# Optimization experiments

Measured on AMD Instinct MI355X. Metric: run time of the kernel, lower is better.

## Reference

```python
import jax, jax.numpy as jnp
import numpy as np

# distilled LLaVA-style decoder: nf4-quantized linears + LoRA(q/k/v/o) + gumbel-softmax -> embedding einsum
B, S, D, H, L = 1, 2048, 2048, 16, 2
DH = D // H
DFF, V, R, BLK = 8192, 32000, 8, 64
LORA_SCALE = 16.0 / R  # alpha / r
TAU = 1.0
SQRT_DH = float(np.sqrt(DH))

# bitsandbytes NF4 codebook (16 values)
NF4 = jnp.array([-1.0, -0.6961928009986877, -0.5250730514526367, -0.39491748809814453,
                 -0.28444138169288635, -0.18477343022823334, -0.09105003625154495, 0.0,
                 0.07958029955625534, 0.16093020141124725, 0.24611230194568634,
                 0.33791524171829224, 0.44070982933044434, 0.5626170039176941,
                 0.7229568362236023, 1.0], dtype=jnp.float32)


def dequant(idx, scale):
    # idx [..., out, in] int in [0,16); scale [..., out, in//BLK] per-block absmax
    return NF4[idx] * jnp.repeat(scale, BLK, axis=-1)


def rmsnorm(x, w):
    return x * jax.lax.rsqrt(jnp.mean(x * x, axis=-1, keepdims=True) + 1e-6) * w


def setup_inputs():
    key = jax.random.key(0)
    k = jax.random.split(key, 12)
    return {
        "input_ids": jax.random.randint(k[0], (B, S), 0, V, dtype=jnp.int32),
        "u": jax.random.uniform(k[1], (B, S, V), dtype=jnp.float32),
        "emb": jax.random.normal(k[2], (V, D), dtype=jnp.float32) * 0.02,
        "attn_scale": jax.random.uniform(k[3], (L, 4, D, D // BLK), minval=0.005, maxval=0.02, dtype=jnp.float32),
        "ffn_gu_scale": jax.random.uniform(k[4], (L, 2, DFF, D // BLK), minval=0.005, maxval=0.02, dtype=jnp.float32),
        "ffn_d_scale": jax.random.uniform(k[5], (L, D, DFF // BLK), minval=0.005, maxval=0.02, dtype=jnp.float32),
        "lora_A": jax.random.normal(k[6], (L, 4, R, D), dtype=jnp.float32) * 0.01,
        "lora_B": jax.random.normal(k[7], (L, 4, D, R), dtype=jnp.float32) * 0.01,
        "norm_w": jnp.ones((L, 2, D), dtype=jnp.float32),
        "final_norm_w": jnp.ones((D,), dtype=jnp.float32),
        "attn_idx": jax.random.randint(k[8], (L, 4, D, D), 0, 16, dtype=jnp.int32),
        "ffn_gu_idx": jax.random.randint(k[9], (L, 2, DFF, D), 0, 16, dtype=jnp.int32),
        "ffn_d_idx": jax.random.randint(k[10], (L, D, DFF), 0, 16, dtype=jnp.int32),
    }


def reference(input_ids, u, emb, attn_scale, ffn_gu_scale, ffn_d_scale,
              lora_A, lora_B, norm_w, final_norm_w, attn_idx, ffn_gu_idx, ffn_d_idx):
    h = emb[input_ids]  # [B, S, D]
    causal = jnp.tril(jnp.ones((S, S), dtype=bool))
    for l in range(L):
        x = rmsnorm(h, norm_w[l, 0])
        w = dequant(attn_idx[l], attn_scale[l])  # [4, D, D] dequantized q/k/v/o weights

        def proj(i, t):
            # nf4 linear + LoRA adapter (y = t W^T + (t A^T) B^T * alpha/r)
            return t @ w[i].T + ((t @ lora_A[l, i].T) @ lora_B[l, i].T) * LORA_SCALE

        q = proj(0, x).reshape(B, S, H, DH)
        k_ = proj(1, x).reshape(B, S, H, DH)
        v = proj(2, x).reshape(B, S, H, DH)
        scores = jnp.einsum('bqhd,bkhd->bhqk', q, k_) / SQRT_DH
        scores = jnp.where(causal, scores, -1e30)
        p = jax.nn.softmax(scores, axis=-1)
        o = jnp.einsum('bhqk,bkhd->bqhd', p, v).reshape(B, S, D)
        h = h + proj(3, o)

        x = rmsnorm(h, norm_w[l, 1])
        wgu = dequant(ffn_gu_idx[l], ffn_gu_scale[l])  # [2, DFF, D] gate/up
        wd = dequant(ffn_d_idx[l], ffn_d_scale[l])     # [D, DFF] down
        h = h + (jax.nn.silu(x @ wgu[0].T) * (x @ wgu[1].T)) @ wd.T

    h = rmsnorm(h, final_norm_w)
    logits = h @ emb.T  # [B, S, V]
    # gumbel_softmax(tau, hard=False): softmax((logits + G)/tau), G = -log(-log(U))
    gnoise = -jnp.log(-jnp.log(u + 1e-10) + 1e-10)
    g = jax.nn.softmax((logits + gnoise) / TAU, axis=-1)
    soft_embeddings = jnp.einsum('bsv,vd->bsd', g, emb)
    return soft_embeddings, logits
```

## Files before the change

### kernel.cpp

```cpp
#include <hip/hip_runtime.h>
#include <hip/hip_bf16.h>

typedef unsigned short u16;
typedef unsigned int u32;
typedef __bf16 bf16t;
typedef bf16t bf16x8 __attribute__((ext_vector_type(8)));
typedef float f32x4 __attribute__((ext_vector_type(4)));

constexpr int S_   = 2048;
constexpr int D_   = 2048;
constexpr int H_   = 16;
constexpr int DH_  = 128;
constexpr int L_   = 2;
constexpr int DFF_ = 8192;
constexpr int V_   = 32000;
constexpr int R_   = 8;

__constant__ float c_nf4[16] = {
  -1.0f, -0.6961928009986877f, -0.5250730514526367f, -0.39491748809814453f,
  -0.28444138169288635f, -0.18477343022823334f, -0.09105003625154495f, 0.0f,
  0.07958029955625534f, 0.16093020141124725f, 0.24611230194568634f,
  0.33791524171829224f, 0.44070982933044434f, 0.5626170039176941f,
  0.7229568362236023f, 1.0f };

__device__ __forceinline__ u16 f2bf(float f) {
  union { float f; u32 u; } v; v.f = f;
  u32 r = v.u + 0x7fffu + ((v.u >> 16) & 1u);
  return (u16)(r >> 16);
}
__device__ __forceinline__ float bf2f(u16 h) {
  union { u32 u; float f; } v; v.u = ((u32)h) << 16; return v.f;
}

__global__ __launch_bounds__(256) void k_gather(const int* __restrict__ ids,
                                                const float* __restrict__ emb,
                                                float* __restrict__ h) {
  int t = blockIdx.x * 256 + threadIdx.x;
  int s = t >> 11;
  int d = t & 2047;
  h[t] = emb[(size_t)ids[s] * D_ + d];
}

__global__ __launch_bounds__(256) void k_rmsnorm(const float* __restrict__ in,
                                                 const float* __restrict__ w,
                                                 u16* __restrict__ out) {
  int s = blockIdx.x;
  const float* x = in + (size_t)s * D_;
  float ss = 0.f;
  for (int d = threadIdx.x; d < D_; d += 256) { float v = x[d]; ss += v * v; }
#pragma unroll
  for (int m = 1; m < 64; m <<= 1) ss += __shfl_xor(ss, m, 64);
  __shared__ float sh[4];
  if ((threadIdx.x & 63) == 0) sh[threadIdx.x >> 6] = ss;
  __syncthreads();
  ss = sh[0] + sh[1] + sh[2] + sh[3];
  float sc = rsqrtf(ss * (1.0f / D_) + 1e-6f);
  u16* o = out + (size_t)s * D_;
  for (int d = threadIdx.x; d < D_; d += 256) o[d] = f2bf(x[d] * sc * w[d]);
}

__global__ __launch_bounds__(256) void k_dequant(const int* __restrict__ idx,
                                                 const float* __restrict__ scale,
                                                 u16* __restrict__ out, int kshift) {
  size_t t = (size_t)blockIdx.x * 256 + threadIdx.x;
  size_t e = t * 8;
  int k = (int)(e & ((1u << kshift) - 1));
  size_t n = e >> kshift;
  float s = scale[(n << (kshift - 6)) + (k >> 6)];
  int4 i0 = *(const int4*)(idx + e);
  int4 i1 = *(const int4*)(idx + e + 4);
  uint4 o;
  o.x = (u32)f2bf(c_nf4[i0.x] * s) | ((u32)f2bf(c_nf4[i0.y] * s) << 16);
  o.y = (u32)f2bf(c_nf4[i0.z] * s) | ((u32)f2bf(c_nf4[i0.w] * s) << 16);
  o.z = (u32)f2bf(c_nf4[i1.x] * s) | ((u32)f2bf(c_nf4[i1.y] * s) << 16);
  o.w = (u32)f2bf(c_nf4[i1.z] * s) | ((u32)f2bf(c_nf4[i1.w] * s) << 16);
  *(uint4*)(out + e) = o;
}

__global__ __launch_bounds__(256) void k_f2b(const float* __restrict__ src,
                                             u16* __restrict__ dst) {
  size_t e = ((size_t)blockIdx.x * 256 + threadIdx.x) * 8;
  float4 f0 = *(const float4*)(src + e);
  float4 f1 = *(const float4*)(src + e + 4);
  uint4 o;
  o.x = (u32)f2bf(f0.x) | ((u32)f2bf(f0.y) << 16);
  o.y = (u32)f2bf(f0.z) | ((u32)f2bf(f0.w) << 16);
  o.z = (u32)f2bf(f1.x) | ((u32)f2bf(f1.y) << 16);
  o.w = (u32)f2bf(f1.z) | ((u32)f2bf(f1.w) << 16);
  *(uint4*)(dst + e) = o;
}

__global__ __launch_bounds__(256) void k_transpose(const float* __restrict__ src,
                                                   u16* __restrict__ dst) {
  __shared__ u16 tile[64][65];
  int v0 = blockIdx.x * 64, d0 = blockIdx.y * 64;
  int tid = threadIdx.x;
  int rr = tid >> 4, cc = (tid & 15) * 4;
#pragma unroll
  for (int j = 0; j < 4; ++j) {
    int r = j * 16 + rr;
    float4 f = *(const float4*)(src + (size_t)(v0 + r) * D_ + d0 + cc);
    tile[r][cc + 0] = f2bf(f.x); tile[r][cc + 1] = f2bf(f.y);
    tile[r][cc + 2] = f2bf(f.z); tile[r][cc + 3] = f2bf(f.w);
  }
  __syncthreads();
#pragma unroll
  for (int j = 0; j < 4; ++j) {
    int r = j * 16 + rr;
    ushort4 w;
    w.x = tile[cc + 0][r]; w.y = tile[cc + 1][r];
    w.z = tile[cc + 2][r]; w.w = tile[cc + 3][r];
    *(ushort4*)(dst + (size_t)(d0 + r) * V_ + v0 + cc) = w;
  }
}

enum { OUT_F32 = 0, OUT_F32_ACC = 1, OUT_BF16 = 2 };

template<int OUTMODE>
__global__ __launch_bounds__(512, 2) void k_gemm256(const u16* __restrict__ A, int lda,
                                                    const u16* __restrict__ B, int ldb,
                                                    void* __restrict__ Cv, int ldc,
                                                    int Kc, size_t zstride) {
  __shared__ u16 As[2][256][64];
  __shared__ u16 Bs[2][256][64];
  const int tid = threadIdx.x;
  const int lane = tid & 63, w = tid >> 6;
  const int wr = w >> 2, wc = w & 3;
  const int g = (lane >> 4), l15 = lane & 15, sl7 = lane & 7;

  const int nbx = gridDim.x;
  const int cpx = (nbx * gridDim.y) >> 3;
  int lin = blockIdx.y * nbx + blockIdx.x;
  int swz = (lin & 7) * cpx + (lin >> 3);
  const int m0 = (swz / nbx) * 256;
  const int n0 = (swz % nbx) * 256;

  A += (size_t)blockIdx.z * Kc;
  B += (size_t)blockIdx.z * Kc;
  float* Cf = (float*)Cv + (size_t)blockIdx.z * zstride;

  const int NT = Kc >> 6;
  const int srow = w * 8 + (lane >> 3);
  const int sch  = (lane & 7) ^ (lane >> 3);

  auto stageA = [&](int half, int tile) {
    const u16* src = A + (size_t)(m0 + half * 128 + srow) * lda + tile * 64 + sch * 8;
    u16* dst = &As[tile & 1][half * 128 + w * 8][0];
#pragma unroll
    for (int rnd = 0; rnd < 2; ++rnd)
      __builtin_amdgcn_global_load_lds(
          (const __attribute__((address_space(1))) void*)(src + (size_t)rnd * 64 * lda),
          (__attribute__((address_space(3))) void*)(dst + rnd * 64 * 64), 16, 0, 0);
  };
  auto stageB = [&](int half, int tile) {
    const u16* src = B + (size_t)(n0 + half * 128 + srow) * ldb + tile * 64 + sch * 8;
    u16* dst = &Bs[tile & 1][half * 128 + w * 8][0];
#pragma unroll
    for (int rnd = 0; rnd < 2; ++rnd)
      __builtin_amdgcn_global_load_lds(
          (const __attribute__((address_space(1))) void*)(src + (size_t)rnd * 64 * ldb),
          (__attribute__((address_space(3))) void*)(dst + rnd * 64 * 64), 16, 0, 0);
  };

  f32x4 acc[8][4] = {};
  bf16x8 areg[4][2], breg[2][2][2];

  stageB(0, 0); stageA(0, 0); stageB(1, 0); stageA(1, 0);
  if (NT > 1) {
    stageB(0, 1); stageA(0, 1);
    asm volatile("s_waitcnt vmcnt(4)" ::: "memory");
  } else {
    asm volatile("s_waitcnt vmcnt(0)" ::: "memory");
  }
  __builtin_amdgcn_s_barrier();

#define LOADA(QR)                                                                   \
  _Pragma("unroll") for (int m = 0; m < 4; ++m)                                     \
    _Pragma("unroll") for (int kh = 0; kh < 2; ++kh) {                              \
      int hr = wr * 128 + (QR) * 64 + m * 16 + l15;                                 \
      areg[m][kh] = *(const bf16x8*)(abase + hr * 64 + ((((kh << 2) | g) ^ sl7) << 3)); \
    }
#define LOADB(QC)                                                                   \
  _Pragma("unroll") for (int n = 0; n < 2; ++n)                                     \
    _Pragma("unroll") for (int kh = 0; kh < 2; ++kh) {                              \
      int br = wc * 64 + (QC) * 32 + n * 16 + l15;                                  \
      breg[QC][n][kh] = *(const bf16x8*)(bbase + br * 64 + ((((kh << 2) | g) ^ sl7) << 3)); \
    }
#define QPHASE(QR, QC)                                                              \
  __builtin_amdgcn_s_setprio(1);                                                    \
  _Pragma("unroll") for (int m = 0; m < 4; ++m)                                     \
    _Pragma("unroll") for (int n = 0; n < 2; ++n)                                   \
      _Pragma("unroll") for (int kh = 0; kh < 2; ++kh)                              \
        acc[(QR) * 4 + m][(QC) * 2 + n] = __builtin_amdgcn_mfma_f32_16x16x32_bf16(  \
            areg[m][kh], breg[QC][n][kh], acc[(QR) * 4 + m][(QC) * 2 + n], 0, 0, 0); \
  __builtin_amdgcn_s_setprio(0);

  for (int t = 0; t < NT; ++t) {
    const u16* abase = &As[t & 1][0][0];
    const u16* bbase = &Bs[t & 1][0][0];
    LOADA(0); LOADB(0);
    if (t + 1 < NT) stageB(1, t + 1);
    QPHASE(0, 0);
    __builtin_amdgcn_s_barrier();
    LOADB(1);
    if (t + 1 < NT) stageA(1, t + 1);
    QPHASE(0, 1);
    __builtin_amdgcn_s_barrier();
    LOADA(1);
    if (t + 2 < NT) stageB(0, t + 2);
    QPHASE(1, 1);
    __builtin_amdgcn_s_barrier();
    if (t + 2 < NT) stageA(0, t + 2);
    QPHASE(1, 0);
    if (t + 1 < NT) {
      if (t + 1 == NT - 1) asm volatile("s_waitcnt vmcnt(0)" ::: "memory");
      else                 asm volatile("s_waitcnt vmcnt(4)" ::: "memory");
    }
    __builtin_amdgcn_s_barrier();
  }
#undef LOADA
#undef LOADB
#undef QPHASE

  const int er = g * 4;
#pragma unroll
  for (int i = 0; i < 8; ++i)
#pragma unroll
    for (int j = 0; j < 4; ++j)
#pragma unroll
      for (int r = 0; r < 4; ++r) {
        int row = m0 + wr * 128 + i * 16 + er + r;
        int col = n0 + wc * 64 + j * 16 + l15;
        if (OUTMODE == OUT_BF16) {
          ((u16*)Cv)[(size_t)row * ldc + col] = f2bf(acc[i][j][r]);
        } else if (OUTMODE == OUT_F32_ACC) {
          Cf[(size_t)row * ldc + col] += acc[i][j][r];
        } else {
          Cf[(size_t)row * ldc + col] = acc[i][j][r];
        }
      }
}

__global__ __launch_bounds__(256) void k_red(const float* __restrict__ P,
                                             float* __restrict__ dst, int accmode) {
  size_t i = ((size_t)blockIdx.x * 256 + threadIdx.x) * 4;
  const size_t n = (size_t)4 * 1024 * 1024;
  float4 a = *(const float4*)(P + i);
  float4 b = *(const float4*)(P + n + i);
  float4 c = *(const float4*)(P + 2 * n + i);
  float4 d = *(const float4*)(P + 3 * n + i);
  float4 r;
  r.x = (a.x + b.x) + (c.x + d.x);
  r.y = (a.y + b.y) + (c.y + d.y);
  r.z = (a.z + b.z) + (c.z + d.z);
  r.w = (a.w + b.w) + (c.w + d.w);
  if (accmode) {
    float4 o = *(const float4*)(dst + i);
    r.x += o.x; r.y += o.y; r.z += o.z; r.w += o.w;
  }
  *(float4*)(dst + i) = r;
}

__global__ __launch_bounds__(256) void k_lora_down(const u16* __restrict__ X,
                                                   const float* __restrict__ A,
                                                   float* __restrict__ T, int nproj) {
  int s = blockIdx.x;
  int lane = threadIdx.x & 63, wv = threadIdx.x >> 6;
  const u16* x = X + (size_t)s * D_;
  for (int p = wv; p < nproj * R_; p += 4) {
    const float* a = A + (size_t)p * D_;
    float sum = 0.f;
    for (int d = lane; d < D_; d += 64) sum += bf2f(x[d]) * a[d];
#pragma unroll
    for (int m = 1; m < 64; m <<= 1) sum += __shfl_xor(sum, m, 64);
    if (lane == 0) T[(size_t)s * (nproj * R_) + p] = sum;
  }
}

__global__ __launch_bounds__(256) void k_lora_up(float* __restrict__ Y, int ystride,
                                                 const float* __restrict__ T,
                                                 const float* __restrict__ Bm, int nproj) {
  int t = blockIdx.x * 256 + threadIdx.x;
  int d = t & (D_ - 1);
  int si = t >> 11;
  int i = si % nproj;
  int s = si / nproj;
  const float* tp = T + ((size_t)s * nproj + i) * R_;
  const float* bp = Bm + ((size_t)i * D_ + d) * R_;
  float acc = 0.f;
#pragma unroll
  for (int r = 0; r < R_; r++) acc += tp[r] * bp[r];
  Y[(size_t)s * ystride + (size_t)i * D_ + d] += 2.0f * acc;
}

__global__ __launch_bounds__(256) void k_attn_mfma(const float* __restrict__ qkv,
                                                   u16* __restrict__ out) {
  __shared__ u16 Ks[64 * 128];
  __shared__ u16 Vs[64 * 128];
  __shared__ u16 PT[4][64 * 16];
  const int tid = threadIdx.x;
  const int lane = tid & 63, w = tid >> 6;
  const int g = lane >> 4, l4 = lane & 15;
  const int q0 = blockIdx.x * 64;
  const int hh = blockIdx.y;
  const int ld = 3 * D_;
  const float rs = 0.08838834764831845f;
  char* ks_base = (char*)Ks;
  char* vs_base = (char*)Vs;
  char* pt_w = (char*)&PT[w][0];

  bf16x8 qf[4];
  const int qglob = q0 + w * 16 + l4;
  {
    const float* qp = qkv + (size_t)qglob * ld + hh * DH_;
#pragma unroll
    for (int kh = 0; kh < 4; ++kh) {
      float4 f0 = *(const float4*)(qp + kh * 32 + g * 8);
      float4 f1 = *(const float4*)(qp + kh * 32 + g * 8 + 4);
      union { bf16x8 v; u16 s[8]; } uq;
      uq.s[0] = f2bf(f0.x); uq.s[1] = f2bf(f0.y); uq.s[2] = f2bf(f0.z); uq.s[3] = f2bf(f0.w);
      uq.s[4] = f2bf(f1.x); uq.s[5] = f2bf(f1.y); uq.s[6] = f2bf(f1.z); uq.s[7] = f2bf(f1.w);
      qf[kh] = uq.v;
    }
  }

  float m = -3.0e38f, lsum = 0.f;
  f32x4 acc_o[8] = {};

  const int nt = blockIdx.x + 1;
  for (int kt = 0; kt < nt; ++kt) {
    const int kv0 = kt * 64;
    __syncthreads();
#pragma unroll
    for (int i = 0; i < 4; ++i) {
      int c = i * 256 + tid;
      int row = c >> 4, cc = c & 15;
      const float* srcK = qkv + (size_t)(kv0 + row) * ld + D_ + hh * DH_ + cc * 8;
      const float* srcV = srcK + D_;
      int byte = row * 256 + cc * 16;
      byte ^= ((row & 7) << 4) ^ (((row >> 3) & 3) << 5);
      {
        float4 f0 = *(const float4*)(srcK);
        float4 f1 = *(const float4*)(srcK + 4);
        uint4 o;
        o.x = (u32)f2bf(f0.x) | ((u32)f2bf(f0.y) << 16);
        o.y = (u32)f2bf(f0.z) | ((u32)f2bf(f0.w) << 16);
        o.z = (u32)f2bf(f1.x) | ((u32)f2bf(f1.y) << 16);
        o.w = (u32)f2bf(f1.z) | ((u32)f2bf(f1.w) << 16);
        *(uint4*)(ks_base + byte) = o;
      }
      {
        float4 f0 = *(const float4*)(srcV);
        float4 f1 = *(const float4*)(srcV + 4);
        uint4 o;
        o.x = (u32)f2bf(f0.x) | ((u32)f2bf(f0.y) << 16);
        o.y = (u32)f2bf(f0.z) | ((u32)f2bf(f0.w) << 16);
        o.z = (u32)f2bf(f1.x) | ((u32)f2bf(f1.y) << 16);
        o.w = (u32)f2bf(f1.z) | ((u32)f2bf(f1.w) << 16);
        *(uint4*)(vs_base + byte) = o;
      }
    }
    __syncthreads();

    f32x4 sa[4] = {};
#pragma unroll
    for (int kb = 0; kb < 4; ++kb) {
#pragma unroll
      for (int kh = 0; kh < 4; ++kh) {
        int key = kb * 16 + l4;
        int byte = key * 256 + kh * 64 + g * 16;
        byte ^= ((key & 7) << 4) ^ (((key >> 3) & 3) << 5);
        bf16x8 af = *(const bf16x8*)(ks_base + byte);
        sa[kb] = __builtin_amdgcn_mfma_f32_16x16x32_bf16(af, qf[kh], sa[kb], 0, 0, 0);
      }
    }

    float p[16];
    float tmax = -3.0e38f;
#pragma unroll
    for (int kb = 0; kb < 4; ++kb)
#pragma unroll
      for (int r = 0; r < 4; ++r) {
        float s = sa[kb][r] * rs;
        int kglob = kv0 + kb * 16 + g * 4 + r;
        if (kglob > qglob) s = -1.0e30f;
        p[kb * 4 + r] = s;
        tmax = fmaxf(tmax, s);
      }
    tmax = fmaxf(tmax, __shfl_xor(tmax, 16, 64));
    tmax = fmaxf(tmax, __shfl_xor(tmax, 32, 64));
    float mnew = fmaxf(m, tmax);
    float corr = __expf(m - mnew);
    m = mnew;
    float psum = 0.f;
#pragma unroll
    for (int i = 0; i < 16; ++i) { p[i] = __expf(p[i] - mnew); psum += p[i]; }
    psum += __shfl_xor(psum, 16, 64);
    psum += __shfl_xor(psum, 32, 64);
    lsum = lsum * corr + psum;
#pragma unroll
    for (int f = 0; f < 8; ++f) {
      acc_o[f][0] *= corr; acc_o[f][1] *= corr;
      acc_o[f][2] *= corr; acc_o[f][3] *= corr;
    }

#pragma unroll
    for (int kb = 0; kb < 4; ++kb)
#pragma unroll
      for (int r = 0; r < 4; ++r) {
        int key = kb * 16 + g * 4 + r;
        int byte = key * 32 + l4 * 2;
        byte ^= ((key >> 3) & 3) << 5;
        *(u16*)(pt_w + byte) = f2bf(p[kb * 4 + r]);
      }

    bf16x8 pb[2];
#pragma unroll
    for (int ks = 0; ks < 2; ++ks) {
      union { bf16x8 v; u16 s[8]; } ub;
#pragma unroll
      for (int j = 0; j < 8; ++j) {
        int key = ks * 32 + g * 8 + j;
        int byte = key * 32 + l4 * 2;
        byte ^= ((key >> 3) & 3) << 5;
        ub.s[j] = *(const u16*)(pt_w + byte);
      }
      pb[ks] = ub.v;
    }
#pragma unroll
    for (int f = 0; f < 8; ++f) {
#pragma unroll
      for (int ks = 0; ks < 2; ++ks) {
        union { bf16x8 v; u16 s[8]; } ua;
#pragma unroll
        for (int j = 0; j < 8; ++j) {
          int key = ks * 32 + g * 8 + j;
          int byte = key * 256 + (f * 16 + l4) * 2;
          byte ^= ((key & 7) << 4) ^ (((key >> 3) & 3) << 5);
          ua.s[j] = *(const u16*)(vs_base + byte);
        }
        acc_o[f] = __builtin_amdgcn_mfma_f32_16x16x32_bf16(ua.v, pb[ks], acc_o[f], 0, 0, 0);
      }
    }
  }

  float inv = 1.f / lsum;
  u16* op = out + (size_t)qglob * D_ + hh * DH_;
#pragma unroll
  for (int f = 0; f < 8; ++f)
#pragma unroll
    for (int r = 0; r < 4; ++r)
      op[f * 16 + g * 4 + r] = f2bf(acc_o[f][r] * inv);
}

__global__ __launch_bounds__(256) void k_silumul(u16* __restrict__ gu) {
  size_t i = ((size_t)blockIdx.x * 256 + threadIdx.x) * 4;
  int s = (int)(i >> 13);
  int f = (int)(i & 8191);
  u16* gp = gu + (size_t)s * (2 * DFF_) + f;
  ushort4 gt = *(ushort4*)gp;
  ushort4 up = *(ushort4*)(gp + DFF_);
  float g0 = bf2f(gt.x), g1 = bf2f(gt.y), g2 = bf2f(gt.z), g3 = bf2f(gt.w);
  float u0 = bf2f(up.x), u1 = bf2f(up.y), u2 = bf2f(up.z), u3 = bf2f(up.w);
  ushort4 o;
  o.x = f2bf(g0 / (1.f + __expf(-g0)) * u0);
  o.y = f2bf(g1 / (1.f + __expf(-g1)) * u1);
  o.z = f2bf(g2 / (1.f + __expf(-g2)) * u2);
  o.w = f2bf(g3 / (1.f + __expf(-g3)) * u3);
  *(ushort4*)gp = o;
}

__global__ __launch_bounds__(256) void k_gumbel(const float* __restrict__ logits,
                                                const float* __restrict__ u,
                                                u16* __restrict__ g) {
  int s = blockIdx.x;
  const float* lp = logits + (size_t)s * V_;
  const float* up = u + (size_t)s * V_;
  float m = -3.0e38f, l = 0.f;
  for (int v = threadIdx.x; v < V_; v += 256) {
    float z = lp[v] - __logf(-__logf(up[v] + 1e-10f) + 1e-10f);
    float mn = fmaxf(m, z);
    l = l * __expf(m - mn) + __expf(z - mn);
    m = mn;
  }
#pragma unroll
  for (int msk = 1; msk < 64; msk <<= 1) {
    float m2 = __shfl_xor(m, msk, 64), l2 = __shfl_xor(l, msk, 64);
    float mn = fmaxf(m, m2);
    l = l * __expf(m - mn) + l2 * __expf(m2 - mn);
    m = mn;
  }
  __shared__ float shm[4], shl[4];
  if ((threadIdx.x & 63) == 0) { shm[threadIdx.x >> 6] = m; shl[threadIdx.x >> 6] = l; }
  __syncthreads();
  float M = fmaxf(fmaxf(shm[0], shm[1]), fmaxf(shm[2], shm[3]));
  float L = shl[0] * __expf(shm[0] - M) + shl[1] * __expf(shm[1] - M) +
            shl[2] * __expf(shm[2] - M) + shl[3] * __expf(shm[3] - M);
  float inv = 1.f / L;
  u16* gp = g + (size_t)s * V_;
  for (int v = threadIdx.x; v < V_; v += 256) {
    float z = lp[v] - __logf(-__logf(up[v] + 1e-10f) + 1e-10f);
    gp[v] = f2bf(__expf(z - M) * inv);
  }
}

extern "C" void kernel_launch(void* const* d_in, const int* in_sizes, int n_in,
                              void* d_out, int out_size, void* d_ws, size_t ws_size,
                              hipStream_t stream) {
  const int*   ids        = (const int*)d_in[0];
  const float* u          = (const float*)d_in[1];
  const float* emb        = (const float*)d_in[2];
  const float* attn_scale = (const float*)d_in[3];
  const float* gu_scale   = (const float*)d_in[4];
  const float* dn_scale   = (const float*)d_in[5];
  const float* lora_A     = (const float*)d_in[6];
  const float* lora_B     = (const float*)d_in[7];
  const float* norm_w     = (const float*)d_in[8];
  const float* fnorm_w    = (const float*)d_in[9];
  const int*   attn_idx   = (const int*)d_in[10];
  const int*   gu_idx     = (const int*)d_in[11];
  const int*   dn_idx     = (const int*)d_in[12];

  float* out_se = (float*)d_out;
  float* out_lg = (float*)d_out + (size_t)S_ * D_;

  char* W = (char*)d_ws;
  float* h    = (float*)(W);
  u16*   xb   = (u16*)(W + ((size_t)16 << 20));
  float* qkv  = (float*)(W + ((size_t)24 << 20));
  u16*   ob   = (u16*)(W + ((size_t)72 << 20));
  u16*   gub  = (u16*)(W + ((size_t)80 << 20));
  u16*   wdq  = (u16*)(W + ((size_t)144 << 20));
  float* Tl   = (float*)(W + ((size_t)208 << 20));
  u16*   embb = (u16*)(W);
  u16*   gsm  = (u16*)(W + ((size_t)125 << 20));
  u16*   embT = (u16*)(W);
  u16*   xbh  = (u16*)d_out;
  float* Pk   = (float*)(W + ((size_t)250 << 20));
  const bool big = ws_size >= ((size_t)314 << 20);
  const size_t ZS = (size_t)4 * 1024 * 1024;

  dim3 b256(256), b512(512);

  k_gather<<<dim3(S_ * D_ / 256), b256, 0, stream>>>(ids, emb, h);

  for (int l = 0; l < L_; ++l) {
    const int*   aidx = attn_idx + (size_t)l * 4 * D_ * D_;
    const float* ascl = attn_scale + (size_t)l * 4 * D_ * (D_ / 64);
    const float* lA   = lora_A + (size_t)l * 4 * R_ * D_;
    const float* lB   = lora_B + (size_t)l * 4 * D_ * R_;

    k_rmsnorm<<<dim3(S_), b256, 0, stream>>>(h, norm_w + (size_t)l * 2 * D_, xb);
    k_dequant<<<dim3(4 * D_ * D_ / 8 / 256), b256, 0, stream>>>(aidx, ascl, wdq, 11);
    k_gemm256<OUT_F32><<<dim3(3 * D_ / 256, 8), b512, 0, stream>>>(
        xb, D_, wdq, D_, qkv, 3 * D_, D_, 0);
    k_lora_down<<<dim3(S_), b256, 0, stream>>>(xb, lA, Tl, 3);
    k_lora_up<<<dim3(S_ * 3 * D_ / 256), b256, 0, stream>>>(qkv, 3 * D_, Tl, lB, 3);
    k_attn_mfma<<<dim3(S_ / 64, H_), b256, 0, stream>>>(qkv, ob);
    k_gemm256<OUT_F32_ACC><<<dim3(D_ / 256, 8), b512, 0, stream>>>(
        ob, D_, wdq + (size_t)3 * D_ * D_, D_, h, D_, D_, 0);
    k_lora_down<<<dim3(S_), b256, 0, stream>>>(ob, lA + (size_t)3 * R_ * D_, Tl, 1);
    k_lora_up<<<dim3(S_ * D_ / 256), b256, 0, stream>>>(h, D_, Tl, lB + (size_t)3 * D_ * R_, 1);

    k_rmsnorm<<<dim3(S_), b256, 0, stream>>>(h, norm_w + (size_t)l * 2 * D_ + D_, xb);
    k_dequant<<<dim3(2 * DFF_ * D_ / 8 / 256), b256, 0, stream>>>(
        gu_idx + (size_t)l * 2 * DFF_ * D_, gu_scale + (size_t)l * 2 * DFF_ * (D_ / 64), wdq, 11);
    k_gemm256<OUT_BF16><<<dim3(2 * DFF_ / 256, 8), b512, 0, stream>>>(
        xb, D_, wdq, D_, gub, 2 * DFF_, D_, 0);
    k_silumul<<<dim3(S_ * DFF_ / 4 / 256), b256, 0, stream>>>(gub);
    k_dequant<<<dim3(D_ * DFF_ / 8 / 256), b256, 0, stream>>>(
        dn_idx + (size_t)l * D_ * DFF_, dn_scale + (size_t)l * D_ * (DFF_ / 64), wdq, 13);
    if (big) {
      k_gemm256<OUT_F32><<<dim3(D_ / 256, 8, 4), b512, 0, stream>>>(
          gub, 2 * DFF_, wdq, DFF_, Pk, D_, DFF_ / 4, ZS);
      k_red<<<dim3(4096), b256, 0, stream>>>(Pk, h, 1);
    } else {
      k_gemm256<OUT_F32_ACC><<<dim3(D_ / 256, 8), b512, 0, stream>>>(
          gub, 2 * DFF_, wdq, DFF_, h, D_, DFF_, 0);
    }
  }

  k_rmsnorm<<<dim3(S_), b256, 0, stream>>>(h, fnorm_w, xbh);
  k_f2b<<<dim3(V_ * D_ / 8 / 256), b256, 0, stream>>>(emb, embb);
  k_gemm256<OUT_F32><<<dim3(V_ / 256, 8), b512, 0, stream>>>(
      xbh, D_, embb, D_, out_lg, V_, D_, 0);
  k_gumbel<<<dim3(S_), b256, 0, stream>>>(out_lg, u, gsm);
  k_transpose<<<dim3(V_ / 64, D_ / 64), b256, 0, stream>>>(emb, embT);
  if (big) {
    k_gemm256<OUT_F32><<<dim3(D_ / 256, 8, 4), b512, 0, stream>>>(
        gsm, V_, embT, V_, Pk, D_, V_ / 4, ZS);
    k_red<<<dim3(4096), b256, 0, stream>>>(Pk, out_se, 0);
  } else {
    k_gemm256<OUT_F32><<<dim3(D_ / 256, 8), b512, 0, stream>>>(
        gsm, V_, embT, V_, out_se, D_, V_, 0);
  }
}
```

Before: 2.870 ms.

## Restructure causal attention with paired query tiles, bf16 QKV, transposed V and async LDS loads

LoRA-up for QKV is fused with conversion to a bf16 QKV buffer, and a separate kernel writes V transposed per head. The attention kernel now processes two query tiles per block (p and 31-p), which balances causal work across blocks and reuses each staged K/V tile for both. K/V tiles are double-buffered into LDS with global_load_lds, and the V operand is read as vector loads instead of scalar gathers. The cost is an extra transpose kernel, extra workspace, higher register pressure, and half as many attention blocks.

```diff
diff --git a/kernel.cpp b/kernel.cpp
--- a/kernel.cpp
+++ b/kernel.cpp
@@ -15,6 +15,8 @@
 constexpr int DFF_ = 8192;
 constexpr int V_   = 32000;
 constexpr int R_   = 8;
+
+#define MFMA16(a, b, c) __builtin_amdgcn_mfma_f32_16x16x32_bf16(a, b, c, 0, 0, 0)
 
 __constant__ float c_nf4[16] = {
   -1.0f, -0.6961928009986877f, -0.5250730514526367f, -0.39491748809814453f,
@@ -293,164 +295,220 @@
   Y[(size_t)s * ystride + (size_t)i * D_ + d] += 2.0f * acc;
 }
 
-__global__ __launch_bounds__(256) void k_attn_mfma(const float* __restrict__ qkv,
-                                                   u16* __restrict__ out) {
-  __shared__ u16 Ks[64 * 128];
-  __shared__ u16 Vs[64 * 128];
+__global__ __launch_bounds__(256) void k_lora_up_qkv(const float* __restrict__ qkv,
+                                                     const float* __restrict__ T,
+                                                     const float* __restrict__ Bm,
+                                                     u16* __restrict__ qkvb) {
+  size_t t = ((size_t)blockIdx.x * 256 + threadIdx.x) * 4;
+  int c = (int)(t % 6144);
+  int s = (int)(t / 6144);
+  int i = c >> 11, d = c & 2047;
+  const float* tp = T + ((size_t)s * 3 + i) * R_;
+  float4 q = *(const float4*)(qkv + t);
+  ushort4 o;
+  float v[4] = {q.x, q.y, q.z, q.w};
+#pragma unroll
+  for (int j = 0; j < 4; ++j) {
+    const float* bp = Bm + ((size_t)i * D_ + d + j) * R_;
+    float acc = 0.f;
+#pragma unroll
+    for (int r = 0; r < R_; r++) acc += tp[r] * bp[r];
+    v[j] += 2.0f * acc;
+  }
+  o.x = f2bf(v[0]); o.y = f2bf(v[1]); o.z = f2bf(v[2]); o.w = f2bf(v[3]);
+  *(ushort4*)(qkvb + t) = o;
+}
+
+__global__ __launch_bounds__(256) void k_vtrans(const u16* __restrict__ qkvb,
+                                                u16* __restrict__ Vt) {
+  __shared__ u16 t[64][136];
+  int s0 = blockIdx.x * 64, hh = blockIdx.y;
+  int tid = threadIdx.x;
+#pragma unroll
+  for (int it = 0; it < 4; ++it) {
+    int e = it * 2048 + tid * 8;
+    int sr = e >> 7, sc = e & 127;
+    *(uint4*)&t[sr][sc] =
+        *(const uint4*)(qkvb + (size_t)(s0 + sr) * 6144 + 4096 + hh * 128 + sc);
+  }
+  __syncthreads();
+#pragma unroll
+  for (int it = 0; it < 4; ++it) {
+    int q = it * 256 + tid;
+    int dh = q >> 3, sc = (q & 7) * 8;
+    u16 e0 = t[sc + 0][dh], e1 = t[sc + 1][dh], e2 = t[sc + 2][dh], e3 = t[sc + 3][dh];
+    u16 e4 = t[sc + 4][dh], e5 = t[sc + 5][dh], e6 = t[sc + 6][dh], e7 = t[sc + 7][dh];
+    uint4 o;
+    o.x = (u32)e0 | ((u32)e1 << 16);
+    o.y = (u32)e2 | ((u32)e3 << 16);
+    o.z = (u32)e4 | ((u32)e5 << 16);
+    o.w = (u32)e6 | ((u32)e7 << 16);
+    *(uint4*)(Vt + ((size_t)hh * DH_ + dh) * S_ + s0 + sc) = o;
+  }
+}
+
+__global__ __launch_bounds__(256) void k_attn2(const u16* __restrict__ qkvb,
+                                               const u16* __restrict__ Vt,
+                                               u16* __restrict__ out) {
+  __shared__ u16 Ks[2][64 * 128];
+  __shared__ u16 VTs[2][128 * 64];
   __shared__ u16 PT[4][64 * 16];
   const int tid = threadIdx.x;
   const int lane = tid & 63, w = tid >> 6;
   const int g = lane >> 4, l4 = lane & 15;
-  const int q0 = blockIdx.x * 64;
+  const int p = blockIdx.x;
   const int hh = blockIdx.y;
-  const int ld = 3 * D_;
+  const int ld = 6144;
   const float rs = 0.08838834764831845f;
-  char* ks_base = (char*)Ks;
-  char* vs_base = (char*)Vs;
+  const int qa0 = p * 64, qb0 = (31 - p) * 64;
+  const int ntb = 32 - p;
   char* pt_w = (char*)&PT[w][0];
 
-  bf16x8 qf[4];
-  const int qglob = q0 + w * 16 + l4;
-  {
-    const float* qp = qkv + (size_t)qglob * ld + hh * DH_;
-#pragma unroll
-    for (int kh = 0; kh < 4; ++kh) {
-      float4 f0 = *(const float4*)(qp + kh * 32 + g * 8);
-      float4 f1 = *(const float4*)(qp + kh * 32 + g * 8 + 4);
-      union { bf16x8 v; u16 s[8]; } uq;
-      uq.s[0] = f2bf(f0.x); uq.s[1] = f2bf(f0.y); uq.s[2] = f2bf(f0.z); uq.s[3] = f2bf(f0.w);
-      uq.s[4] = f2bf(f1.x); uq.s[5] = f2bf(f1.y); uq.s[6] = f2bf(f1.z); uq.s[7] = f2bf(f1.w);
-      qf[kh] = uq.v;
-    }
-  }
-
-  float m = -3.0e38f, lsum = 0.f;
-  f32x4 acc_o[8] = {};
-
-  const int nt = blockIdx.x + 1;
-  for (int kt = 0; kt < nt; ++kt) {
+  const int qga = qa0 + w * 16 + l4;
+  const int qgb = qb0 + w * 16 + l4;
+
+  bf16x8 qfa[4], qfb[4];
+#pragma unroll
+  for (int kh = 0; kh < 4; ++kh) {
+    qfa[kh] = *(const bf16x8*)(qkvb + (size_t)qga * ld + hh * DH_ + kh * 32 + g * 8);
+    qfb[kh] = *(const bf16x8*)(qkvb + (size_t)qgb * ld + hh * DH_ + kh * 32 + g * 8);
+  }
+
+  float ma = -3.0e38f, la = 0.f, mb = -3.0e38f, lb = 0.f;
+  f32x4 acc_a[8] = {}, acc_b[8] = {};
+  bf16x8 pba[2], pbb[2];
+
+  auto stage = [&](int buf, int kt) {
     const int kv0 = kt * 64;
-    __syncthreads();
 #pragma unroll
     for (int i = 0; i < 4; ++i) {
-      int c = i * 256 + tid;
-      int row = c >> 4, cc = c & 15;
-      const float* srcK = qkv + (size_t)(kv0 + row) * ld + D_ + hh * DH_ + cc * 8;
-      const float* srcV = srcK + D_;
-      int byte = row * 256 + cc * 16;
-      byte ^= ((row & 7) << 4) ^ (((row >> 3) & 3) << 5);
-      {
-        float4 f0 = *(const float4*)(srcK);
-        float4 f1 = *(const float4*)(srcK + 4);
-        uint4 o;
-        o.x = (u32)f2bf(f0.x) | ((u32)f2bf(f0.y) << 16);
-        o.y = (u32)f2bf(f0.z) | ((u32)f2bf(f0.w) << 16);
-        o.z = (u32)f2bf(f1.x) | ((u32)f2bf(f1.y) << 16);
-        o.w = (u32)f2bf(f1.z) | ((u32)f2bf(f1.w) << 16);
-        *(uint4*)(ks_base + byte) = o;
-      }
-      {
-        float4 f0 = *(const float4*)(srcV);
-        float4 f1 = *(const float4*)(srcV + 4);
-        uint4 o;
-        o.x = (u32)f2bf(f0.x) | ((u32)f2bf(f0.y) << 16);
-        o.y = (u32)f2bf(f0.z) | ((u32)f2bf(f0.w) << 16);
-        o.z = (u32)f2bf(f1.x) | ((u32)f2bf(f1.y) << 16);
-        o.w = (u32)f2bf(f1.z) | ((u32)f2bf(f1.w) << 16);
-        *(uint4*)(vs_base + byte) = o;
-      }
-    }
-    __syncthreads();
-
-    f32x4 sa[4] = {};
-#pragma unroll
-    for (int kb = 0; kb < 4; ++kb) {
-#pragma unroll
-      for (int kh = 0; kh < 4; ++kh) {
-        int key = kb * 16 + l4;
-        int byte = key * 256 + kh * 64 + g * 16;
-        byte ^= ((key & 7) << 4) ^ (((key >> 3) & 3) << 5);
-        bf16x8 af = *(const bf16x8*)(ks_base + byte);
-        sa[kb] = __builtin_amdgcn_mfma_f32_16x16x32_bf16(af, qf[kh], sa[kb], 0, 0, 0);
-      }
-    }
-
-    float p[16];
+      int rl = (w * 4 + i) * 4 + (lane >> 4);
+      int cs = (lane & 15) ^ ((rl & 7) ^ (((rl >> 3) & 3) << 1));
+      __builtin_amdgcn_global_load_lds(
+          (const __attribute__((address_space(1))) void*)(
+              qkvb + (size_t)(kv0 + rl) * ld + 2048 + hh * DH_ + cs * 8),
+          (__attribute__((address_space(3))) void*)(&Ks[buf][(w * 4 + i) * 512]), 16, 0, 0);
+    }
+#pragma unroll
+    for (int i = 0; i < 4; ++i) {
+      int dh = (w * 4 + i) * 8 + (lane >> 3);
+      int cs = (lane & 7) ^ (dh & 7);
+      __builtin_amdgcn_global_load_lds(
+          (const __attribute__((address_space(1))) void*)(
+              Vt + ((size_t)hh * DH_ + dh) * S_ + kv0 + cs * 8),
+          (__attribute__((address_space(3))) void*)(&VTs[buf][(w * 4 + i) * 512]), 16, 0, 0);
+    }
+  };
+
+  auto softpb = [&](f32x4* sv, float& m, float& l, f32x4* acc, int qg, bool diag,
+                    int kv0, bf16x8* pb) {
+    float pv[16];
     float tmax = -3.0e38f;
 #pragma unroll
     for (int kb = 0; kb < 4; ++kb)
 #pragma unroll
       for (int r = 0; r < 4; ++r) {
-        float s = sa[kb][r] * rs;
-        int kglob = kv0 + kb * 16 + g * 4 + r;
-        if (kglob > qglob) s = -1.0e30f;
-        p[kb * 4 + r] = s;
+        float s = sv[kb][r] * rs;
+        if (diag) {
+          int kglob = kv0 + kb * 16 + g * 4 + r;
+          if (kglob > qg) s = -1.0e30f;
+        }
+        pv[kb * 4 + r] = s;
         tmax = fmaxf(tmax, s);
       }
     tmax = fmaxf(tmax, __shfl_xor(tmax, 16, 64));
     tmax = fmaxf(tmax, __shfl_xor(tmax, 32, 64));
-    float mnew = fmaxf(m, tmax);
-    float corr = __expf(m - mnew);
-    m = mnew;
-    float psum = 0.f;
-#pragma unroll
-    for (int i = 0; i < 16; ++i) { p[i] = __expf(p[i] - mnew); psum += p[i]; }
-    psum += __shfl_xor(psum, 16, 64);
-    psum += __shfl_xor(psum, 32, 64);
-    lsum = lsum * corr + psum;
+    float mn = fmaxf(m, tmax);
+    float corr = __expf(m - mn);
+    m = mn;
+    float ps = 0.f;
+#pragma unroll
+    for (int i = 0; i < 16; ++i) { pv[i] = __expf(pv[i] - mn); ps += pv[i]; }
+    ps += __shfl_xor(ps, 16, 64);
+    ps += __shfl_xor(ps, 32, 64);
+    l = l * corr + ps;
 #pragma unroll
     for (int f = 0; f < 8; ++f) {
-      acc_o[f][0] *= corr; acc_o[f][1] *= corr;
-      acc_o[f][2] *= corr; acc_o[f][3] *= corr;
-    }
-
+      acc[f][0] *= corr; acc[f][1] *= corr; acc[f][2] *= corr; acc[f][3] *= corr;
+    }
 #pragma unroll
     for (int kb = 0; kb < 4; ++kb)
 #pragma unroll
       for (int r = 0; r < 4; ++r) {
         int key = kb * 16 + g * 4 + r;
-        int byte = key * 32 + l4 * 2;
-        byte ^= ((key >> 3) & 3) << 5;
-        *(u16*)(pt_w + byte) = f2bf(p[kb * 4 + r]);
+        int byte = (key * 32 + l4 * 2) ^ (((key >> 3) & 3) << 5);
+        *(u16*)(pt_w + byte) = f2bf(pv[kb * 4 + r]);
       }
-
-    bf16x8 pb[2];
 #pragma unroll
     for (int ks = 0; ks < 2; ++ks) {
       union { bf16x8 v; u16 s[8]; } ub;
 #pragma unroll
       for (int j = 0; j < 8; ++j) {
         int key = ks * 32 + g * 8 + j;
-        int byte = key * 32 + l4 * 2;
-        byte ^= ((key >> 3) & 3) << 5;
+        int byte = (key * 32 + l4 * 2) ^ (((key >> 3) & 3) << 5);
         ub.s[j] = *(const u16*)(pt_w + byte);
       }
       pb[ks] = ub.v;
     }
+  };
+
+  stage(0, 0);
+  asm volatile("s_waitcnt vmcnt(0)" ::: "memory");
+  __syncthreads();
+
+  for (int kt = 0; kt < ntb; ++kt) {
+    const int kv0 = kt * 64;
+    const int buf = kt & 1;
+    if (kt + 1 < ntb) stage(buf ^ 1, kt + 1);
+
+    const char* kb_base = (const char*)&Ks[buf][0];
+    const char* vb_base = (const char*)&VTs[buf][0];
+    const bool doa = (kt <= p);
+
+    f32x4 sa[4] = {}, sb[4] = {};
+#pragma unroll
+    for (int kb = 0; kb < 4; ++kb) {
+#pragma unroll
+      for (int kh = 0; kh < 4; ++kh) {
+        int key = kb * 16 + l4;
+        int ch = (kh * 4 + g) ^ ((key & 7) ^ (((key >> 3) & 3) << 1));
+        bf16x8 af = *(const bf16x8*)(kb_base + key * 256 + ch * 16);
+        if (doa) sa[kb] = MFMA16(af, qfa[kh], sa[kb]);
+        sb[kb] = MFMA16(af, qfb[kh], sb[kb]);
+      }
+    }
+
+    if (doa) softpb(sa, ma, la, acc_a, qga, kt == p, kv0, pba);
+    softpb(sb, mb, lb, acc_b, qgb, kt == ntb - 1, kv0, pbb);
+
 #pragma unroll
     for (int f = 0; f < 8; ++f) {
 #pragma unroll
       for (int ks = 0; ks < 2; ++ks) {
-        union { bf16x8 v; u16 s[8]; } ua;
-#pragma unroll
-        for (int j = 0; j < 8; ++j) {
-          int key = ks * 32 + g * 8 + j;
-          int byte = key * 256 + (f * 16 + l4) * 2;
-          byte ^= ((key & 7) << 4) ^ (((key >> 3) & 3) << 5);
-          ua.s[j] = *(const u16*)(vs_base + byte);
-        }
-        acc_o[f] = __builtin_amdgcn_mfma_f32_16x16x32_bf16(ua.v, pb[ks], acc_o[f], 0, 0, 0);
+        int dh = f * 16 + l4;
+        int ch = (ks * 4 + g) ^ (dh & 7);
+        bf16x8 va = *(const bf16x8*)(vb_base + dh * 128 + ch * 16);
+        if (doa) acc_a[f] = MFMA16(va, pba[ks], acc_a[f]);
+        acc_b[f] = MFMA16(va, pbb[ks], acc_b[f]);
       }
     }
-  }
-
-  float inv = 1.f / lsum;
-  u16* op = out + (size_t)qglob * D_ + hh * DH_;
+
+    if (kt + 1 < ntb) {
+      asm volatile("s_waitcnt vmcnt(0)" ::: "memory");
+      __syncthreads();
+    }
+  }
+
+  float inva = 1.f / la, invb = 1.f / lb;
+  u16* opa = out + (size_t)qga * D_ + hh * DH_;
+  u16* opb = out + (size_t)qgb * D_ + hh * DH_;
 #pragma unroll
   for (int f = 0; f < 8; ++f)
 #pragma unroll
-    for (int r = 0; r < 4; ++r)
-      op[f * 16 + g * 4 + r] = f2bf(acc_o[f][r] * inv);
+    for (int r = 0; r < 4; ++r) {
+      opa[f * 16 + g * 4 + r] = f2bf(acc_a[f][r] * inva);
+      opb[f * 16 + g * 4 + r] = f2bf(acc_b[f][r] * invb);
+    }
 }
 
 __global__ __launch_bounds__(256) void k_silumul(u16* __restrict__ gu) {
@@ -528,10 +586,12 @@
   float* h    = (float*)(W);
   u16*   xb   = (u16*)(W + ((size_t)16 << 20));
   float* qkv  = (float*)(W + ((size_t)24 << 20));
-  u16*   ob   = (u16*)(W + ((size_t)72 << 20));
-  u16*   gub  = (u16*)(W + ((size_t)80 << 20));
-  u16*   wdq  = (u16*)(W + ((size_t)144 << 20));
-  float* Tl   = (float*)(W + ((size_t)208 << 20));
+  u16*   qkvb = (u16*)(W + ((size_t)72 << 20));
+  u16*   Vtb  = (u16*)(W + ((size_t)96 << 20));
+  u16*   ob   = (u16*)(W + ((size_t)104 << 20));
+  u16*   gub  = (u16*)(W + ((size_t)112 << 20));
+  u16*   wdq  = (u16*)(W + ((size_t)176 << 20));
+  float* Tl   = (float*)(W + ((size_t)240 << 20));
   u16*   embb = (u16*)(W);
   u16*   gsm  = (u16*)(W + ((size_t)125 << 20));
   u16*   embT = (u16*)(W);
@@ -555,8 +615,9 @@
     k_gemm256<OUT_F32><<<dim3(3 * D_ / 256, 8), b512, 0, stream>>>(
         xb, D_, wdq, D_, qkv, 3 * D_, D_, 0);
     k_lora_down<<<dim3(S_), b256, 0, stream>>>(xb, lA, Tl, 3);
-    k_lora_up<<<dim3(S_ * 3 * D_ / 256), b256, 0, stream>>>(qkv, 3 * D_, Tl, lB, 3);
-    k_attn_mfma<<<dim3(S_ / 64, H_), b256, 0, stream>>>(qkv, ob);
+    k_lora_up_qkv<<<dim3(S_ * 3 * D_ / 4 / 256), b256, 0, stream>>>(qkv, Tl, lB, qkvb);
+    k_vtrans<<<dim3(S_ / 64, H_), b256, 0, stream>>>(qkvb, Vtb);
+    k_attn2<<<dim3(16, H_), b256, 0, stream>>>(qkvb, Vtb, ob);
     k_gemm256<OUT_F32_ACC><<<dim3(D_ / 256, 8), b512, 0, stream>>>(
         ob, D_, wdq + (size_t)3 * D_ * D_, D_, h, D_, D_, 0);
     k_lora_down<<<dim3(S_), b256, 0, stream>>>(ob, lA + (size_t)3 * R_ * D_, Tl, 1);
```

New measurement: 2.493 ms. 13.2% less time.
